# Performance work log

Hardware: AMD Instinct MI355X
Metric: run time of the kernel (lower is better)

The kernel has to match this reference:

```python
import jax, jax.numpy as jnp
import numpy as np

D = 512
H = 8
DH = D // H
DFF = 2048
SLOTS = 1024
TOPK = 5
LN_EPS = 1e-5
NORM_EPS = 1e-12


def setup_inputs() -> dict:
    key = jax.random.key(0)
    ks = jax.random.split(key, 12)
    B, S = 8, 1024
    inp = {
        "src": jax.random.normal(ks[0], (B, S, D), dtype=jnp.float32),
        # MultiheadAttention params (torch layout: in_proj [3D, D], out_proj [D, D])
        "in_proj_w": jax.random.normal(ks[1], (3 * D, D), dtype=jnp.float32) * 0.02,
        "in_proj_b": jnp.zeros((3 * D,), dtype=jnp.float32),
        "out_proj_w": jax.random.normal(ks[2], (D, D), dtype=jnp.float32) * 0.02,
        "out_proj_b": jnp.zeros((D,), dtype=jnp.float32),
        # BPBookMemory params
        "memory": jax.random.normal(ks[3], (SLOTS, D), dtype=jnp.float32),
        "retrieval_scale": jnp.asarray(0.1, dtype=jnp.float32),
        # LayerNorms
        "ln1_g": jnp.ones((D,), dtype=jnp.float32),
        "ln1_b": jnp.zeros((D,), dtype=jnp.float32),
        "ln2_g": jnp.ones((D,), dtype=jnp.float32),
        "ln2_b": jnp.zeros((D,), dtype=jnp.float32),
        # FFN (torch Linear layout: [out, in])
        "w1": jax.random.normal(ks[4], (DFF, D), dtype=jnp.float32) * 0.02,
        "b1": jnp.zeros((DFF,), dtype=jnp.float32),
        "w2": jax.random.normal(ks[5], (D, DFF), dtype=jnp.float32) * 0.02,
        "b2": jnp.zeros((D,), dtype=jnp.float32),
    }
    return inp


def _layer_norm(x, g, b):
    mu = jnp.mean(x, axis=-1, keepdims=True)
    var = jnp.var(x, axis=-1, keepdims=True)
    return (x - mu) * jax.lax.rsqrt(var + LN_EPS) * g + b


def _l2_normalize(x):
    n = jnp.linalg.norm(x, axis=-1, keepdims=True)
    return x / jnp.maximum(n, NORM_EPS)


def _forward(src, in_proj_w, in_proj_b, out_proj_w, out_proj_b,
             memory, retrieval_scale, ln1_g, ln1_b, ln2_g, ln2_b,
             w1, b1, w2, b2):
    B, S, _ = src.shape
    # ---- pre-norm self-attention ----
    h = _layer_norm(src, ln1_g, ln1_b)
    qkv = h @ in_proj_w.T + in_proj_b            # [B,S,3D]
    q, k, v = jnp.split(qkv, 3, axis=-1)
    q = q.reshape(B, S, H, DH)
    k = k.reshape(B, S, H, DH)
    v = v.reshape(B, S, H, DH)
    scores = jnp.einsum("bqhd,bkhd->bhqk", q, k) / jnp.sqrt(jnp.float32(DH))
    attn = jax.nn.softmax(scores, axis=-1)
    ctx = jnp.einsum("bhqk,bkhd->bqhd", attn, v).reshape(B, S, D)
    attn_out = ctx @ out_proj_w.T + out_proj_b
    src = src + attn_out
    # ---- BP-Book memory: cosine sim -> topk -> softmax -> gather -> weighted sum ----
    xn = _l2_normalize(src)                      # [B,S,D]
    mn = _l2_normalize(memory)                   # [SLOTS,D]
    sim = xn @ mn.T                              # [B,S,SLOTS]
    topk_scores, topk_idx = jax.lax.top_k(sim, TOPK)
    w = jax.nn.softmax(topk_scores, axis=-1)     # [B,S,TOPK]
    retrieved = memory[topk_idx]                 # [B,S,TOPK,D]
    weighted = jnp.einsum("bskd,bsk->bsd", retrieved, w)
    src = src + retrieval_scale * weighted
    # ---- FFN ----
    h = _layer_norm(src, ln2_g, ln2_b)
    ffn = jax.nn.gelu(h @ w1.T + b1, approximate=False) @ w2.T + b2
    return src + ffn


def reference(src, in_proj_w, in_proj_b, out_proj_w, out_proj_b,
              memory, retrieval_scale, ln1_g, ln1_b, ln2_g, ln2_b,
              w1, b1, w2, b2):
    return _forward(src, in_proj_w, in_proj_b, out_proj_w, out_proj_b,
                    memory, retrieval_scale, ln1_g, ln1_b, ln2_g, ln2_b,
                    w1, b1, w2, b2)
```

## Files before the change

kernel.cpp:

```cpp
#include <hip/hip_runtime.h>
#include <math.h>

#define D_ 512
#define H_ 8
#define DFF_ 2048
#define SLOTS_ 1024
#define TOPK_ 5
#define NCAND_ 8
#define NTOK_ 8192
#define SEQ_ 1024
#define LN_EPS_ 1e-5f

typedef __attribute__((ext_vector_type(8))) short bf16x8;
typedef __attribute__((ext_vector_type(4))) float f32x4;
typedef __attribute__((ext_vector_type(4))) unsigned u32x4;
typedef unsigned short u16;

__device__ inline void split2(float x, unsigned short& hi, unsigned short& lo) {
    unsigned u = __builtin_bit_cast(unsigned, x);
    hi = (unsigned short)(u >> 16);
    float h = __builtin_bit_cast(float, u & 0xFFFF0000u);
    float rem = x - h;
    lo = (unsigned short)(__builtin_bit_cast(unsigned, rem) >> 16);
}

__device__ __forceinline__ void gld16(const void* g, void* l) {
    __builtin_amdgcn_global_load_lds(
        (const __attribute__((address_space(1))) void*)g,
        (__attribute__((address_space(3))) void*)l, 16, 0, 0);
}

__device__ __forceinline__ int SW7(int r) { return (r ^ (r >> 3)) & 7; }
__device__ __forceinline__ const bf16x8* frag(const unsigned short* p, int r, int c) {
    return (const bf16x8*)(p + r * 64 + ((c ^ SW7(r)) << 3));
}

__global__ __launch_bounds__(256) void prep_kernel(
    const float* __restrict__ inw, const float* __restrict__ outw,
    const float* __restrict__ w1, const float* __restrict__ w2,
    const float* __restrict__ mem, const float* __restrict__ src,
    const float* __restrict__ ln1g, const float* __restrict__ ln1b,
    u16* __restrict__ inwh, u16* __restrict__ inwl,
    u16* __restrict__ outwh, u16* __restrict__ outwl,
    u16* __restrict__ w1h, u16* __restrict__ w2h,
    float* __restrict__ mn, u16* __restrict__ mnh, u16* __restrict__ mnl,
    u16* __restrict__ hh, u16* __restrict__ hl)
{
    const int bid = blockIdx.x;
    const int t = threadIdx.x;
    if (bid < 3072) {
        const int i = (bid * 256 + t) * 4;
        const float* x;
        u16 *hhp, *llp;
        int base;
        if (i < 786432)       { x = inw;  hhp = inwh;  llp = inwl;  base = 0; }
        else if (i < 1048576) { x = outw; hhp = outwh; llp = outwl; base = 786432; }
        else if (i < 2097152) { x = w1;   hhp = w1h;   llp = nullptr; base = 1048576; }
        else                  { x = w2;   hhp = w2h;   llp = nullptr; base = 2097152; }
        const int j = i - base;
        const float4 v = *(const float4*)(x + j);
        const float vv[4] = {v.x, v.y, v.z, v.w};
        u16 h[4], l[4];
#pragma unroll
        for (int e = 0; e < 4; ++e) split2(vv[e], h[e], l[e]);
        hhp[j + 0] = h[0]; hhp[j + 1] = h[1]; hhp[j + 2] = h[2]; hhp[j + 3] = h[3];
        if (llp) { llp[j + 0] = l[0]; llp[j + 1] = l[1]; llp[j + 2] = l[2]; llp[j + 3] = l[3]; }
    } else if (bid < 3328) {
        const int row = (bid - 3072) * 4 + (t >> 6);
        const int lane = t & 63;
        float v[8];
        float ss = 0.0f;
#pragma unroll
        for (int j = 0; j < 8; ++j) {
            v[j] = mem[(size_t)row * D_ + j * 64 + lane];
            ss += v[j] * v[j];
        }
#pragma unroll
        for (int off = 32; off; off >>= 1) ss += __shfl_xor(ss, off);
        const float inv = 1.0f / fmaxf(sqrtf(ss), 1e-12f);
#pragma unroll
        for (int j = 0; j < 8; ++j) {
            const float y = v[j] * inv;
            mn[(size_t)row * D_ + j * 64 + lane] = y;
            u16 h, l;
            split2(y, h, l);
            mnh[(size_t)row * D_ + j * 64 + lane] = h;
            mnl[(size_t)row * D_ + j * 64 + lane] = l;
        }
    } else {
        const int row = bid - 3328;
        const float a = src[(size_t)row * D_ + t];
        const float b = src[(size_t)row * D_ + t + 256];
        float s = a + b;
        float ss = a * a + b * b;
#pragma unroll
        for (int off = 32; off; off >>= 1) {
            s += __shfl_xor(s, off);
            ss += __shfl_xor(ss, off);
        }
        __shared__ float rs[4], rss[4];
        if ((t & 63) == 0) { rs[t >> 6] = s; rss[t >> 6] = ss; }
        __syncthreads();
        s = rs[0] + rs[1] + rs[2] + rs[3];
        ss = rss[0] + rss[1] + rss[2] + rss[3];
        const float mu = s * (1.0f / D_);
        const float var = ss * (1.0f / D_) - mu * mu;
        const float r = rsqrtf(var + LN_EPS_);
        const float y0 = (a - mu) * r * ln1g[t] + ln1b[t];
        const float y1 = (b - mu) * r * ln1g[t + 256] + ln1b[t + 256];
        u16 h0, l0, h1, l1;
        split2(y0, h0, l0);
        split2(y1, h1, l1);
        hh[(size_t)row * D_ + t] = h0;
        hh[(size_t)row * D_ + t + 256] = h1;
        hl[(size_t)row * D_ + t] = l0;
        hl[(size_t)row * D_ + t + 256] = l1;
    }
}

enum { EP_QKV = 0, EP_OUTPROJ = 1, EP_SIM = 2, EP_FFN1 = 3, EP_FFN2 = 4 };

template <int SPLIT, int MODE>
__global__ __launch_bounds__(256) void gemm_mf(
    const unsigned short* __restrict__ Ahg, const unsigned short* __restrict__ Alg,
    const unsigned short* __restrict__ Bhg, const unsigned short* __restrict__ Blg,
    const float* __restrict__ bias, const float* __restrict__ res,
    float* __restrict__ C,
    unsigned short* __restrict__ Ch, unsigned short* __restrict__ Cl,
    int M, int N, int K)
{
    __shared__ __align__(16) unsigned short sm[(SPLIT == 3 ? 4 : 2) * 8192];
    unsigned short* Ah = sm;
    unsigned short* Al = sm + 8192;
    unsigned short* Bh = sm + (SPLIT == 3 ? 16384 : 8192);
    unsigned short* Bl = sm + 24576;

    const int tid = threadIdx.x;
    const int lane = tid & 63;
    const int w = tid >> 6;
    const int wr = w >> 1, wc = w & 1;
    const int g = lane >> 4, ln = lane & 15;
    const int m0 = blockIdx.x * 128, n0 = blockIdx.y * 128;
    const int lrow8 = lane >> 3, lchunk = lane & 7;

    const unsigned short* gsrc;
    unsigned short* lds;
    int rbase, rofs, nblk;
    if (SPLIT == 3) {
        nblk = 16; rofs = 0;
        if (w == 0)      { gsrc = Ahg; lds = Ah; rbase = m0; }
        else if (w == 1) { gsrc = Alg; lds = Al; rbase = m0; }
        else if (w == 2) { gsrc = Bhg; lds = Bh; rbase = n0; }
        else             { gsrc = Blg; lds = Bl; rbase = n0; }
    } else {
        nblk = 8; rofs = (w & 1) * 64;
        if (w < 2) { gsrc = Ahg; lds = Ah; rbase = m0; }
        else       { gsrc = Bhg; lds = Bh; rbase = n0; }
    }

    f32x4 acc[4][4];
#pragma unroll
    for (int i = 0; i < 4; ++i)
#pragma unroll
        for (int j = 0; j < 4; ++j) acc[i][j] = (f32x4){0.f, 0.f, 0.f, 0.f};

    for (int k0 = 0; k0 < K; k0 += 64) {
#pragma unroll
        for (int blk = 0; blk < nblk; ++blk) {
            const int row = rofs + blk * 8 + lrow8;
            const int sc = lchunk ^ SW7(row);
            gld16(gsrc + (size_t)(rbase + row) * K + k0 + sc * 8,
                  lds + (rofs + blk * 8) * 64);
        }
        __syncthreads();

#pragma unroll
        for (int ks = 0; ks < 2; ++ks) {
            bf16x8 a_h[4], a_l[4], b_h[4], b_l[4];
#pragma unroll
            for (int mi = 0; mi < 4; ++mi) {
                a_h[mi] = *frag(Ah, wr * 64 + mi * 16 + ln, ks * 4 + g);
                if (SPLIT == 3) a_l[mi] = *frag(Al, wr * 64 + mi * 16 + ln, ks * 4 + g);
            }
#pragma unroll
            for (int ni = 0; ni < 4; ++ni) {
                b_h[ni] = *frag(Bh, wc * 64 + ni * 16 + ln, ks * 4 + g);
                if (SPLIT == 3) b_l[ni] = *frag(Bl, wc * 64 + ni * 16 + ln, ks * 4 + g);
            }
#pragma unroll
            for (int mi = 0; mi < 4; ++mi)
#pragma unroll
                for (int ni = 0; ni < 4; ++ni) {
                    acc[mi][ni] = __builtin_amdgcn_mfma_f32_16x16x32_bf16(
                        a_h[mi], b_h[ni], acc[mi][ni], 0, 0, 0);
                    if (SPLIT == 3) {
                        acc[mi][ni] = __builtin_amdgcn_mfma_f32_16x16x32_bf16(
                            a_h[mi], b_l[ni], acc[mi][ni], 0, 0, 0);
                        acc[mi][ni] = __builtin_amdgcn_mfma_f32_16x16x32_bf16(
                            a_l[mi], b_h[ni], acc[mi][ni], 0, 0, 0);
                    }
                }
        }
        __syncthreads();
    }

#pragma unroll
    for (int mi = 0; mi < 4; ++mi) {
#pragma unroll
        for (int ni = 0; ni < 4; ++ni) {
            const int gn = n0 + wc * 64 + ni * 16 + ln;
            const float bz = (MODE == EP_SIM) ? 0.0f : bias[gn];
#pragma unroll
            for (int r2 = 0; r2 < 4; ++r2) {
                const int gm = m0 + wr * 64 + mi * 16 + g * 4 + r2;
                float v = acc[mi][ni][r2];
                if (MODE == EP_SIM) {
                    C[(size_t)gm * N + gn] = v;
                } else if (MODE == EP_QKV) {
                    v += bz;
                    if (gn < D_) v *= 0.125f;
                    unsigned short h16, l16;
                    split2(v, h16, l16);
                    Ch[(size_t)gm * N + gn] = h16;
                    Cl[(size_t)gm * N + gn] = l16;
                } else if (MODE == EP_OUTPROJ) {
                    v += bz + res[(size_t)gm * N + gn];
                    C[(size_t)gm * N + gn] = v;
                    unsigned short h16, l16;
                    split2(v, h16, l16);
                    Ch[(size_t)gm * N + gn] = h16;
                } else if (MODE == EP_FFN1) {
                    v += bz;
                    v = 0.5f * v * (1.0f + erff(v * 0.70710678118654752f));
                    unsigned short h16, l16;
                    split2(v, h16, l16);
                    Ch[(size_t)gm * N + gn] = h16;
                } else {
                    v += bz + res[(size_t)gm * N + gn];
                    C[(size_t)gm * N + gn] = v;
                }
            }
        }
    }
}

__global__ __launch_bounds__(256, 2) void attn_kernel(
    const unsigned short* __restrict__ qkvh, const unsigned short* __restrict__ qkvl,
    unsigned short* __restrict__ ctxh, unsigned short* __restrict__ ctxl)
{
    const int id = blockIdx.x;
    const int bh = id & 63;
    const int qt = id >> 6;
    const int b = bh >> 3, h = bh & 7;
    const int tok0 = b * SEQ_ + qt * 128;
    const int kbase0 = b * SEQ_;
    const int tid = threadIdx.x;
    const int lane = tid & 63;
    const int w = tid >> 6;
    const int ln = lane & 15, g = lane >> 4;
    const int lrow8 = lane >> 3, lchunk = lane & 7;

    __shared__ __align__(16) unsigned char smb[65536];
    unsigned*       PP  = (unsigned*)smb;
    unsigned short* Qh  = (unsigned short*)smb;
    unsigned short* Ql  = (unsigned short*)(smb + 16384);
    unsigned short* Kh  = (unsigned short*)(smb + 32768);
    unsigned short* Kl  = (unsigned short*)(smb + 40960);
    unsigned short* Vth = (unsigned short*)(smb + 49152);
    unsigned short* Vtl = (unsigned short*)(smb + 57344);

    const int qoff = h * 64, koff = 512 + h * 64, voff = 1024 + h * 64;

#pragma unroll
    for (int blk = 0; blk < 4; ++blk) {
        const int row = w * 32 + blk * 8 + lrow8;
        const int sc = lchunk ^ SW7(row);
        gld16(qkvh + (size_t)(tok0 + row) * 1536 + qoff + sc * 8,
              Qh + (w * 32 + blk * 8) * 64);
        gld16(qkvl + (size_t)(tok0 + row) * 1536 + qoff + sc * 8,
              Ql + (w * 32 + blk * 8) * 64);
    }
    __syncthreads();
    bf16x8 qfh[2][2], qfl[2][2];
#pragma unroll
    for (int qi = 0; qi < 2; ++qi)
#pragma unroll
        for (int ks = 0; ks < 2; ++ks) {
            qfh[qi][ks] = *frag(Qh, w * 32 + qi * 16 + ln, ks * 4 + g);
            qfl[qi][ks] = *frag(Ql, w * 32 + qi * 16 + ln, ks * 4 + g);
        }
    __syncthreads();

    f32x4 o[4][2];
#pragma unroll
    for (int di = 0; di < 4; ++di)
#pragma unroll
        for (int qi = 0; qi < 2; ++qi) o[di][qi] = (f32x4){0.f, 0.f, 0.f, 0.f};
    float mrow2[2] = {-INFINITY, -INFINITY};
    float lrow2[2] = {0.f, 0.f};

    const int p2 = tid & 31, dc = tid >> 5;

    for (int kt = 0; kt < 16; ++kt) {
        const int kb2 = kbase0 + kt * 64;
#pragma unroll
        for (int blk = 0; blk < 2; ++blk) {
            const int row = w * 16 + blk * 8 + lrow8;
            const int sc = lchunk ^ SW7(row);
            gld16(qkvh + (size_t)(kb2 + row) * 1536 + koff + sc * 8,
                  Kh + (w * 16 + blk * 8) * 64);
            gld16(qkvl + (size_t)(kb2 + row) * 1536 + koff + sc * 8,
                  Kl + (w * 16 + blk * 8) * 64);
        }
        {
            const size_t b0 = (size_t)(kb2 + 2 * p2) * 1536 + voff + dc * 8;
            const bf16x8 h0 = *(const bf16x8*)(qkvh + b0);
            const bf16x8 h1 = *(const bf16x8*)(qkvh + b0 + 1536);
            const bf16x8 l0 = *(const bf16x8*)(qkvl + b0);
            const bf16x8 l1 = *(const bf16x8*)(qkvl + b0 + 1536);
#pragma unroll
            for (int j = 0; j < 8; ++j) {
                const int d = dc * 8 + j;
                const int idx = d * 64 + (((p2 >> 2) ^ SW7(d)) << 3) + ((p2 & 3) << 1);
                *(unsigned*)&Vth[idx] = (unsigned)(unsigned short)h0[j]
                                      | ((unsigned)(unsigned short)h1[j] << 16);
                *(unsigned*)&Vtl[idx] = (unsigned)(unsigned short)l0[j]
                                      | ((unsigned)(unsigned short)l1[j] << 16);
            }
        }
        __syncthreads();

        f32x4 s[4][2];
#pragma unroll
        for (int ki = 0; ki < 4; ++ki)
#pragma unroll
            for (int qi = 0; qi < 2; ++qi) s[ki][qi] = (f32x4){0.f, 0.f, 0.f, 0.f};
        __builtin_amdgcn_s_setprio(1);
#pragma unroll
        for (int ks = 0; ks < 2; ++ks) {
            bf16x8 kbh[4], kbl[4];
#pragma unroll
            for (int ki = 0; ki < 4; ++ki) {
                kbh[ki] = *frag(Kh, ki * 16 + ln, ks * 4 + g);
                kbl[ki] = *frag(Kl, ki * 16 + ln, ks * 4 + g);
            }
#pragma unroll
            for (int ki = 0; ki < 4; ++ki)
#pragma unroll
                for (int qi = 0; qi < 2; ++qi) {
                    s[ki][qi] = __builtin_amdgcn_mfma_f32_16x16x32_bf16(kbh[ki], qfh[qi][ks], s[ki][qi], 0, 0, 0);
                    s[ki][qi] = __builtin_amdgcn_mfma_f32_16x16x32_bf16(kbh[ki], qfl[qi][ks], s[ki][qi], 0, 0, 0);
                    s[ki][qi] = __builtin_amdgcn_mfma_f32_16x16x32_bf16(kbl[ki], qfh[qi][ks], s[ki][qi], 0, 0, 0);
                }
        }
        __builtin_amdgcn_s_setprio(0);

        float tm2[2], alpha2[2], psum2[2];
#pragma unroll
        for (int qi = 0; qi < 2; ++qi) {
            float m01 = fmaxf(fmaxf(s[0][qi][0], s[0][qi][1]), fmaxf(s[0][qi][2], s[0][qi][3]));
            float m23 = fmaxf(fmaxf(s[1][qi][0], s[1][qi][1]), fmaxf(s[1][qi][2], s[1][qi][3]));
            float m45 = fmaxf(fmaxf(s[2][qi][0], s[2][qi][1]), fmaxf(s[2][qi][2], s[2][qi][3]));
            float m67 = fmaxf(fmaxf(s[3][qi][0], s[3][qi][1]), fmaxf(s[3][qi][2], s[3][qi][3]));
            tm2[qi] = fmaxf(fmaxf(m01, m23), fmaxf(m45, m67));
        }
#pragma unroll
        for (int qi = 0; qi < 2; ++qi) {
            tm2[qi] = fmaxf(tm2[qi], __shfl_xor(tm2[qi], 16));
            tm2[qi] = fmaxf(tm2[qi], __shfl_xor(tm2[qi], 32));
            const float mnew = fmaxf(mrow2[qi], tm2[qi]);
            alpha2[qi] = __expf(mrow2[qi] - mnew);
            mrow2[qi] = mnew;
            psum2[qi] = 0.f;
        }
#pragma unroll
        for (int qi = 0; qi < 2; ++qi)
#pragma unroll
            for (int ki = 0; ki < 4; ++ki) {
                u32x4 pv;
#pragma unroll
                for (int r2 = 0; r2 < 4; ++r2) {
                    const float p = __expf(s[ki][qi][r2] - mrow2[qi]);
                    psum2[qi] += p;
                    unsigned short h16, l16;
                    split2(p, h16, l16);
                    pv[r2] = (unsigned)h16 | ((unsigned)l16 << 16);
                }
                *(u32x4*)&PP[(w * 32 + qi * 16 + ln) * 64 + (((ki * 4 + g) ^ (ln & 7)) << 2)] = pv;
            }
#pragma unroll
        for (int qi = 0; qi < 2; ++qi) {
            psum2[qi] += __shfl_xor(psum2[qi], 16);
            psum2[qi] += __shfl_xor(psum2[qi], 32);
            lrow2[qi] = lrow2[qi] * alpha2[qi] + psum2[qi];
        }
#pragma unroll
        for (int di = 0; di < 4; ++di)
#pragma unroll
            for (int qi = 0; qi < 2; ++qi)
#pragma unroll
                for (int r2 = 0; r2 < 4; ++r2)
                    o[di][qi][r2] *= alpha2[qi];

        __builtin_amdgcn_s_setprio(1);
#pragma unroll
        for (int ks = 0; ks < 2; ++ks) {
            bf16x8 pah[2], pal[2];
#pragma unroll
            for (int qi = 0; qi < 2; ++qi) {
                const unsigned* rowp = PP + (w * 32 + qi * 16 + ln) * 64;
                const int c0 = (2 * ks + (g >> 1)) * 4 + (g & 1) * 2;
                const u32x4 q0 = *(const u32x4*)(rowp + (((c0    ) ^ (ln & 7)) << 2));
                const u32x4 q1 = *(const u32x4*)(rowp + (((c0 + 1) ^ (ln & 7)) << 2));
                u32x4 hu, lu;
                hu[0] = __builtin_amdgcn_perm(q0[1], q0[0], 0x05040100u);
                hu[1] = __builtin_amdgcn_perm(q0[3], q0[2], 0x05040100u);
                hu[2] = __builtin_amdgcn_perm(q1[1], q1[0], 0x05040100u);
                hu[3] = __builtin_amdgcn_perm(q1[3], q1[2], 0x05040100u);
                lu[0] = __builtin_amdgcn_perm(q0[1], q0[0], 0x07060302u);
                lu[1] = __builtin_amdgcn_perm(q0[3], q0[2], 0x07060302u);
                lu[2] = __builtin_amdgcn_perm(q1[1], q1[0], 0x07060302u);
                lu[3] = __builtin_amdgcn_perm(q1[3], q1[2], 0x07060302u);
                pah[qi] = __builtin_bit_cast(bf16x8, hu);
                pal[qi] = __builtin_bit_cast(bf16x8, lu);
            }
            bf16x8 vbh[4], vbl[4];
#pragma unroll
            for (int di = 0; di < 4; ++di) {
                vbh[di] = *frag(Vth, di * 16 + ln, ks * 4 + g);
                vbl[di] = *frag(Vtl, di * 16 + ln, ks * 4 + g);
            }
#pragma unroll
            for (int di = 0; di < 4; ++di)
#pragma unroll
                for (int qi = 0; qi < 2; ++qi) {
                    o[di][qi] = __builtin_amdgcn_mfma_f32_16x16x32_bf16(vbh[di], pah[qi], o[di][qi], 0, 0, 0);
                    o[di][qi] = __builtin_amdgcn_mfma_f32_16x16x32_bf16(vbh[di], pal[qi], o[di][qi], 0, 0, 0);
                    o[di][qi] = __builtin_amdgcn_mfma_f32_16x16x32_bf16(vbl[di], pah[qi], o[di][qi], 0, 0, 0);
                }
        }
        __builtin_amdgcn_s_setprio(0);
        __syncthreads();
    }

#pragma unroll
    for (int di = 0; di < 4; ++di)
#pragma unroll
        for (int qi = 0; qi < 2; ++qi) {
            const float inv = 1.0f / lrow2[qi];
            u32x4 tv;
#pragma unroll
            for (int r2 = 0; r2 < 4; ++r2) {
                const float v = o[di][qi][r2] * inv;
                unsigned short h16, l16;
                split2(v, h16, l16);
                tv[r2] = (unsigned)h16 | ((unsigned)l16 << 16);
            }
            *(u32x4*)&PP[(w * 32 + qi * 16 + ln) * 64 + (((di * 4 + g) ^ (ln & 7)) << 2)] = tv;
        }
    __syncthreads();
    {
        const int qrow = lane >> 1, halfd = lane & 1;
        const unsigned* rowp = PP + (w * 32 + qrow) * 64;
        const size_t gbase = (size_t)(tok0 + w * 32 + qrow) * D_ + h * 64;
#pragma unroll
        for (int gi = 0; gi < 2; ++gi) {
            const int di = halfd * 2 + gi;
#pragma unroll
            for (int pr = 0; pr < 2; ++pr) {
                const int c = di * 4 + pr * 2;
                const u32x4 t0 = *(const u32x4*)(rowp + (((c    ) ^ (qrow & 7)) << 2));
                const u32x4 t1 = *(const u32x4*)(rowp + (((c + 1) ^ (qrow & 7)) << 2));
                u32x4 hv, lv;
                hv[0] = __builtin_amdgcn_perm(t0[1], t0[0], 0x05040100u);
                hv[1] = __builtin_amdgcn_perm(t0[3], t0[2], 0x05040100u);
                hv[2] = __builtin_amdgcn_perm(t1[1], t1[0], 0x05040100u);
                hv[3] = __builtin_amdgcn_perm(t1[3], t1[2], 0x05040100u);
                lv[0] = __builtin_amdgcn_perm(t0[1], t0[0], 0x07060302u);
                lv[1] = __builtin_amdgcn_perm(t0[3], t0[2], 0x07060302u);
                lv[2] = __builtin_amdgcn_perm(t1[1], t1[0], 0x07060302u);
                lv[3] = __builtin_amdgcn_perm(t1[3], t1[2], 0x07060302u);
                *(u32x4*)(ctxh + gbase + di * 16 + pr * 8) = hv;
                *(u32x4*)(ctxl + gbase + di * 16 + pr * 8) = lv;
            }
        }
    }
}

__global__ __launch_bounds__(64) void topk_kernel(
    const float* __restrict__ sim, const float* __restrict__ src2,
    const float* __restrict__ mn, const float* __restrict__ mem,
    const float* __restrict__ rs_ptr, const float* __restrict__ g2,
    const float* __restrict__ b2, float* __restrict__ out,
    unsigned short* __restrict__ h2h)
{
    const int row = blockIdx.x;
    const int lane = threadIdx.x;
    float v[16];
#pragma unroll
    for (int j = 0; j < 16; ++j)
        v[j] = sim[(size_t)row * SLOTS_ + j * 64 + lane];

    int ci[NCAND_];
#pragma unroll
    for (int t = 0; t < NCAND_; ++t) {
        float bv = -INFINITY;
        int bi = 0x7fffffff;
#pragma unroll
        for (int j = 0; j < 16; ++j) {
            const int idx = j * 64 + lane;
            if (v[j] > bv) { bv = v[j]; bi = idx; }
        }
#pragma unroll
        for (int off = 32; off; off >>= 1) {
            const float ov = __shfl_xor(bv, off);
            const int oi = __shfl_xor(bi, off);
            if (ov > bv || (ov == bv && oi < bi)) { bv = ov; bi = oi; }
        }
        ci[t] = bi;
#pragma unroll
        for (int j = 0; j < 16; ++j)
            if (j * 64 + lane == bi) v[j] = -INFINITY;
    }

    float x[8];
    float ss = 0.0f;
#pragma unroll
    for (int j = 0; j < 8; ++j) {
        x[j] = src2[(size_t)row * D_ + j * 64 + lane];
        ss += x[j] * x[j];
    }
#pragma unroll
    for (int off = 32; off; off >>= 1) ss += __shfl_xor(ss, off);
    const float invn = 1.0f / fmaxf(sqrtf(ss), 1e-12f);

    float rv[NCAND_];
#pragma unroll
    for (int t = 0; t < NCAND_; ++t) {
        const float* mrow = mn + (size_t)ci[t] * D_;
        float acc = 0.0f;
#pragma unroll
        for (int j = 0; j < 8; ++j)
            acc = fmaf(x[j], mrow[j * 64 + lane], acc);
#pragma unroll
        for (int off = 32; off; off >>= 1) acc += __shfl_xor(acc, off);
        rv[t] = acc * invn;
    }

    float wv[TOPK_];
    int wi[TOPK_];
    bool used[NCAND_];
#pragma unroll
    for (int t = 0; t < NCAND_; ++t) used[t] = false;
#pragma unroll
    for (int t = 0; t < TOPK_; ++t) {
        float bv = -INFINITY;
        int bi = 0x7fffffff, bu = 0;
#pragma unroll
        for (int u = 0; u < NCAND_; ++u) {
            if (!used[u] && (rv[u] > bv || (rv[u] == bv && ci[u] < bi))) {
                bv = rv[u]; bi = ci[u]; bu = u;
            }
        }
        used[bu] = true;
        wv[t] = bv;
        wi[t] = bi;
    }

    float m = wv[0];
#pragma unroll
    for (int t = 1; t < TOPK_; ++t) m = fmaxf(m, wv[t]);
    float w[TOPK_], ssum = 0.0f;
#pragma unroll
    for (int t = 0; t < TOPK_; ++t) { w[t] = __expf(wv[t] - m); ssum += w[t]; }
    const float scale = rs_ptr[0] / ssum;

    float y[8];
    float s_ = 0.f, ss2 = 0.f;
#pragma unroll
    for (int j = 0; j < 8; ++j) {
        const int d = j * 64 + lane;
        float acc = 0.0f;
#pragma unroll
        for (int t = 0; t < TOPK_; ++t)
            acc += w[t] * mem[(size_t)wi[t] * D_ + d];
        y[j] = x[j] + scale * acc;
        out[(size_t)row * D_ + d] = y[j];
        s_ += y[j];
        ss2 += y[j] * y[j];
    }
#pragma unroll
    for (int off = 32; off; off >>= 1) {
        s_ += __shfl_xor(s_, off);
        ss2 += __shfl_xor(ss2, off);
    }
    const float mu = s_ * (1.0f / D_);
    const float var = ss2 * (1.0f / D_) - mu * mu;
    const float r = rsqrtf(var + LN_EPS_);
#pragma unroll
    for (int j = 0; j < 8; ++j) {
        const int d = j * 64 + lane;
        const float h2 = (y[j] - mu) * r * g2[d] + b2[d];
        unsigned short h16, l16;
        split2(h2, h16, l16);
        h2h[(size_t)row * D_ + d] = h16;
    }
}

extern "C" void kernel_launch(void* const* d_in, const int* in_sizes, int n_in,
                              void* d_out, int out_size, void* d_ws, size_t ws_size,
                              hipStream_t stream)
{
    const float* src  = (const float*)d_in[0];
    const float* inw  = (const float*)d_in[1];
    const float* inb  = (const float*)d_in[2];
    const float* outw = (const float*)d_in[3];
    const float* outb = (const float*)d_in[4];
    const float* mem  = (const float*)d_in[5];
    const float* rs   = (const float*)d_in[6];
    const float* ln1g = (const float*)d_in[7];
    const float* ln1b = (const float*)d_in[8];
    const float* ln2g = (const float*)d_in[9];
    const float* ln2b = (const float*)d_in[10];
    const float* w1   = (const float*)d_in[11];
    const float* b1   = (const float*)d_in[12];
    const float* w2   = (const float*)d_in[13];
    const float* b2   = (const float*)d_in[14];
    float* out = (float*)d_out;
    char* ws = (char*)d_ws;
    const size_t MB = 1024ull * 1024ull;

    float* mn   = (float*)(ws + 0);
    u16* mnh    = (u16*)(ws + 2 * MB);
    u16* mnl    = (u16*)(ws + 3 * MB);
    u16* h2h    = (u16*)(ws + 4 * MB);
    u16* inwh   = (u16*)(ws + 4 * MB);
    u16* inwl   = (u16*)(ws + 5 * MB + 512 * 1024);
    u16* outwh  = (u16*)(ws + 7 * MB);
    u16* outwl  = (u16*)(ws + 7 * MB + 512 * 1024);
    u16* w1h    = (u16*)(ws + 77 * MB);
    u16* w2h    = (u16*)(ws + 79 * MB);
    u16* hh     = (u16*)(ws + 13 * MB);
    u16* hl     = (u16*)(ws + 21 * MB);
    u16* qkvh   = (u16*)(ws + 29 * MB);
    u16* qkvl   = (u16*)(ws + 53 * MB);
    u16* ctxh   = (u16*)(ws + 13 * MB);
    u16* ctxl   = (u16*)(ws + 21 * MB);
    float* sim  = (float*)(ws + 13 * MB);
    float* src2 = (float*)(ws + 45 * MB);
    u16* src2h  = (u16*)(ws + 61 * MB);
    u16* Gbf    = (u16*)(ws + 21 * MB);

    prep_kernel<<<dim3(11520), dim3(256), 0, stream>>>(
        inw, outw, w1, w2, mem, src, ln1g, ln1b,
        inwh, inwl, outwh, outwl, w1h, w2h, mn, mnh, mnl, hh, hl);
    gemm_mf<3, EP_QKV><<<dim3(64, 12), dim3(256), 0, stream>>>(
        hh, hl, inwh, inwl, inb, nullptr, nullptr, qkvh, qkvl, NTOK_, 1536, 512);
    attn_kernel<<<dim3(512), dim3(256), 0, stream>>>(qkvh, qkvl, ctxh, ctxl);
    gemm_mf<3, EP_OUTPROJ><<<dim3(64, 4), dim3(256), 0, stream>>>(
        ctxh, ctxl, outwh, outwl, outb, src, src2, src2h, nullptr, NTOK_, 512, 512);
    gemm_mf<1, EP_SIM><<<dim3(64, 8), dim3(256), 0, stream>>>(
        src2h, nullptr, mnh, nullptr, nullptr, nullptr, sim, nullptr, nullptr, NTOK_, 1024, 512);
    topk_kernel<<<dim3(NTOK_), dim3(64), 0, stream>>>(
        sim, src2, mn, mem, rs, ln2g, ln2b, out, h2h);
    gemm_mf<1, EP_FFN1><<<dim3(64, 16), dim3(256), 0, stream>>>(
        h2h, nullptr, w1h, nullptr, b1, nullptr, nullptr, Gbf, nullptr, NTOK_, 2048, 512);
    gemm_mf<1, EP_FFN2><<<dim3(64, 4), dim3(256), 0, stream>>>(
        Gbf, nullptr, w2h, nullptr, b2, out, out, nullptr, nullptr, NTOK_, 512, 2048);
}
```

Baseline: 282.9 us.

## Load GEMM B and attention K fragments directly from global into registers

The GEMM kernel stops staging the B operand (weights) in LDS. Each wave now loads its B MFMA fragments straight from global memory into registers, which halves LDS use and frees all four waves to load A. The attention kernel does the same for the K tiles, cutting its LDS footprint from 64KB to 48KB. The topk kernel packs four rows per 256-thread block. The intent is to raise occupancy and cut LDS traffic, at the cost of uncoalesced, redundant global loads (each wave row re-reads B) and higher register pressure.

```diff
diff --git a/kernel.cpp b/kernel.cpp
--- a/kernel.cpp
+++ b/kernel.cpp
@@ -129,11 +129,9 @@
     unsigned short* __restrict__ Ch, unsigned short* __restrict__ Cl,
     int M, int N, int K)
 {
-    __shared__ __align__(16) unsigned short sm[(SPLIT == 3 ? 4 : 2) * 8192];
+    __shared__ __align__(16) unsigned short sm[(SPLIT == 3 ? 2 : 1) * 8192];
     unsigned short* Ah = sm;
     unsigned short* Al = sm + 8192;
-    unsigned short* Bh = sm + (SPLIT == 3 ? 16384 : 8192);
-    unsigned short* Bl = sm + 24576;
 
     const int tid = threadIdx.x;
     const int lane = tid & 63;
@@ -145,18 +143,18 @@
 
     const unsigned short* gsrc;
     unsigned short* lds;
-    int rbase, rofs, nblk;
+    int rofs, nblk;
     if (SPLIT == 3) {
-        nblk = 16; rofs = 0;
-        if (w == 0)      { gsrc = Ahg; lds = Ah; rbase = m0; }
-        else if (w == 1) { gsrc = Alg; lds = Al; rbase = m0; }
-        else if (w == 2) { gsrc = Bhg; lds = Bh; rbase = n0; }
-        else             { gsrc = Blg; lds = Bl; rbase = n0; }
+        gsrc = (w >= 2) ? Alg : Ahg;
+        lds  = (w >= 2) ? Al  : Ah;
+        rofs = (w & 1) * 64;
+        nblk = 8;
     } else {
-        nblk = 8; rofs = (w & 1) * 64;
-        if (w < 2) { gsrc = Ahg; lds = Ah; rbase = m0; }
-        else       { gsrc = Bhg; lds = Bh; rbase = n0; }
-    }
+        gsrc = Ahg; lds = Ah; rofs = w * 32; nblk = 4;
+    }
+
+    const unsigned short* bph = Bhg + (size_t)(n0 + wc * 64 + ln) * K;
+    const unsigned short* bpl = (SPLIT == 3) ? (Blg + (size_t)(n0 + wc * 64 + ln) * K) : nullptr;
 
     f32x4 acc[4][4];
 #pragma unroll
@@ -165,39 +163,43 @@
         for (int j = 0; j < 4; ++j) acc[i][j] = (f32x4){0.f, 0.f, 0.f, 0.f};
 
     for (int k0 = 0; k0 < K; k0 += 64) {
+        bf16x8 bg_h[2][4], bg_l[2][4];
+#pragma unroll
+        for (int ks = 0; ks < 2; ++ks)
+#pragma unroll
+            for (int ni = 0; ni < 4; ++ni) {
+                bg_h[ks][ni] = *(const bf16x8*)(bph + (size_t)ni * 16 * K + k0 + (ks * 4 + g) * 8);
+                if (SPLIT == 3)
+                    bg_l[ks][ni] = *(const bf16x8*)(bpl + (size_t)ni * 16 * K + k0 + (ks * 4 + g) * 8);
+            }
 #pragma unroll
         for (int blk = 0; blk < nblk; ++blk) {
             const int row = rofs + blk * 8 + lrow8;
             const int sc = lchunk ^ SW7(row);
-            gld16(gsrc + (size_t)(rbase + row) * K + k0 + sc * 8,
+            gld16(gsrc + (size_t)(m0 + row) * K + k0 + sc * 8,
                   lds + (rofs + blk * 8) * 64);
         }
         __syncthreads();
 
 #pragma unroll
         for (int ks = 0; ks < 2; ++ks) {
-            bf16x8 a_h[4], a_l[4], b_h[4], b_l[4];
+            bf16x8 a_h[4], a_l[4];
 #pragma unroll
             for (int mi = 0; mi < 4; ++mi) {
                 a_h[mi] = *frag(Ah, wr * 64 + mi * 16 + ln, ks * 4 + g);
                 if (SPLIT == 3) a_l[mi] = *frag(Al, wr * 64 + mi * 16 + ln, ks * 4 + g);
             }
 #pragma unroll
-            for (int ni = 0; ni < 4; ++ni) {
-                b_h[ni] = *frag(Bh, wc * 64 + ni * 16 + ln, ks * 4 + g);
-                if (SPLIT == 3) b_l[ni] = *frag(Bl, wc * 64 + ni * 16 + ln, ks * 4 + g);
-            }
-#pragma unroll
             for (int mi = 0; mi < 4; ++mi)
 #pragma unroll
                 for (int ni = 0; ni < 4; ++ni) {
                     acc[mi][ni] = __builtin_amdgcn_mfma_f32_16x16x32_bf16(
-                        a_h[mi], b_h[ni], acc[mi][ni], 0, 0, 0);
+                        a_h[mi], bg_h[ks][ni], acc[mi][ni], 0, 0, 0);
                     if (SPLIT == 3) {
                         acc[mi][ni] = __builtin_amdgcn_mfma_f32_16x16x32_bf16(
-                            a_h[mi], b_l[ni], acc[mi][ni], 0, 0, 0);
+                            a_h[mi], bg_l[ks][ni], acc[mi][ni], 0, 0, 0);
                         acc[mi][ni] = __builtin_amdgcn_mfma_f32_16x16x32_bf16(
-                            a_l[mi], b_h[ni], acc[mi][ni], 0, 0, 0);
+                            a_l[mi], bg_h[ks][ni], acc[mi][ni], 0, 0, 0);
                     }
                 }
         }
@@ -260,14 +262,12 @@
     const int ln = lane & 15, g = lane >> 4;
     const int lrow8 = lane >> 3, lchunk = lane & 7;
 
-    __shared__ __align__(16) unsigned char smb[65536];
+    __shared__ __align__(16) unsigned char smb[49152];
     unsigned*       PP  = (unsigned*)smb;
     unsigned short* Qh  = (unsigned short*)smb;
     unsigned short* Ql  = (unsigned short*)(smb + 16384);
-    unsigned short* Kh  = (unsigned short*)(smb + 32768);
-    unsigned short* Kl  = (unsigned short*)(smb + 40960);
-    unsigned short* Vth = (unsigned short*)(smb + 49152);
-    unsigned short* Vtl = (unsigned short*)(smb + 57344);
+    unsigned short* Vth = (unsigned short*)(smb + 32768);
+    unsigned short* Vtl = (unsigned short*)(smb + 40960);
 
     const int qoff = h * 64, koff = 512 + h * 64, voff = 1024 + h * 64;
 
@@ -300,18 +300,20 @@
     float lrow2[2] = {0.f, 0.f};
 
     const int p2 = tid & 31, dc = tid >> 5;
+    const unsigned short* kph = qkvh + (size_t)(kbase0 + ln) * 1536 + koff + g * 8;
+    const unsigned short* kpl = qkvl + (size_t)(kbase0 + ln) * 1536 + koff + g * 8;
 
     for (int kt = 0; kt < 16; ++kt) {
         const int kb2 = kbase0 + kt * 64;
-#pragma unroll
-        for (int blk = 0; blk < 2; ++blk) {
-            const int row = w * 16 + blk * 8 + lrow8;
-            const int sc = lchunk ^ SW7(row);
-            gld16(qkvh + (size_t)(kb2 + row) * 1536 + koff + sc * 8,
-                  Kh + (w * 16 + blk * 8) * 64);
-            gld16(qkvl + (size_t)(kb2 + row) * 1536 + koff + sc * 8,
-                  Kl + (w * 16 + blk * 8) * 64);
-        }
+        bf16x8 kgh[2][4], kgl[2][4];
+#pragma unroll
+        for (int ks = 0; ks < 2; ++ks)
+#pragma unroll
+            for (int ki = 0; ki < 4; ++ki) {
+                const size_t ofs = ((size_t)kt * 64 + ki * 16) * 1536 + ks * 32;
+                kgh[ks][ki] = *(const bf16x8*)(kph + ofs);
+                kgl[ks][ki] = *(const bf16x8*)(kpl + ofs);
+            }
         {
             const size_t b0 = (size_t)(kb2 + 2 * p2) * 1536 + voff + dc * 8;
             const bf16x8 h0 = *(const bf16x8*)(qkvh + b0);
@@ -337,22 +339,15 @@
             for (int qi = 0; qi < 2; ++qi) s[ki][qi] = (f32x4){0.f, 0.f, 0.f, 0.f};
         __builtin_amdgcn_s_setprio(1);
 #pragma unroll
-        for (int ks = 0; ks < 2; ++ks) {
-            bf16x8 kbh[4], kbl[4];
-#pragma unroll
-            for (int ki = 0; ki < 4; ++ki) {
-                kbh[ki] = *frag(Kh, ki * 16 + ln, ks * 4 + g);
-                kbl[ki] = *frag(Kl, ki * 16 + ln, ks * 4 + g);
-            }
+        for (int ks = 0; ks < 2; ++ks)
 #pragma unroll
             for (int ki = 0; ki < 4; ++ki)
 #pragma unroll
                 for (int qi = 0; qi < 2; ++qi) {
-                    s[ki][qi] = __builtin_amdgcn_mfma_f32_16x16x32_bf16(kbh[ki], qfh[qi][ks], s[ki][qi], 0, 0, 0);
-                    s[ki][qi] = __builtin_amdgcn_mfma_f32_16x16x32_bf16(kbh[ki], qfl[qi][ks], s[ki][qi], 0, 0, 0);
-                    s[ki][qi] = __builtin_amdgcn_mfma_f32_16x16x32_bf16(kbl[ki], qfh[qi][ks], s[ki][qi], 0, 0, 0);
+                    s[ki][qi] = __builtin_amdgcn_mfma_f32_16x16x32_bf16(kgh[ks][ki], qfh[qi][ks], s[ki][qi], 0, 0, 0);
+                    s[ki][qi] = __builtin_amdgcn_mfma_f32_16x16x32_bf16(kgh[ks][ki], qfl[qi][ks], s[ki][qi], 0, 0, 0);
+                    s[ki][qi] = __builtin_amdgcn_mfma_f32_16x16x32_bf16(kgl[ks][ki], qfh[qi][ks], s[ki][qi], 0, 0, 0);
                 }
-        }
         __builtin_amdgcn_s_setprio(0);
 
         float tm2[2], alpha2[2], psum2[2];
@@ -487,15 +482,15 @@
     }
 }
 
-__global__ __launch_bounds__(64) void topk_kernel(
+__global__ __launch_bounds__(256) void topk_kernel(
     const float* __restrict__ sim, const float* __restrict__ src2,
     const float* __restrict__ mn, const float* __restrict__ mem,
     const float* __restrict__ rs_ptr, const float* __restrict__ g2,
     const float* __restrict__ b2, float* __restrict__ out,
     unsigned short* __restrict__ h2h)
 {
-    const int row = blockIdx.x;
-    const int lane = threadIdx.x;
+    const int row = blockIdx.x * 4 + (threadIdx.x >> 6);
+    const int lane = threadIdx.x & 63;
     float v[16];
 #pragma unroll
     for (int j = 0; j < 16; ++j)
@@ -661,7 +656,7 @@
         ctxh, ctxl, outwh, outwl, outb, src, src2, src2h, nullptr, NTOK_, 512, 512);
     gemm_mf<1, EP_SIM><<<dim3(64, 8), dim3(256), 0, stream>>>(
         src2h, nullptr, mnh, nullptr, nullptr, nullptr, sim, nullptr, nullptr, NTOK_, 1024, 512);
-    topk_kernel<<<dim3(NTOK_), dim3(64), 0, stream>>>(
+    topk_kernel<<<dim3(2048), dim3(256), 0, stream>>>(
         sim, src2, mn, mem, rs, ln2g, ln2b, out, h2h);
     gemm_mf<1, EP_FFN1><<<dim3(64, 16), dim3(256), 0, stream>>>(
         h2h, nullptr, w1h, nullptr, b1, nullptr, nullptr, Gbf, nullptr, NTOK_, 2048, 512);
```

After: 404.6 us. 43.0% more time.
